# Kernel optimization log

Hardware: AMD Instinct MI355X
Metric: run time of the kernel (lower is better)

## Reference

```python
import jax, jax.numpy as jnp
import numpy as np

B, S, D, H = 2, 2048, 2048, 16
HD = D // H
RESIDUAL_SCALE = 1.0
EPS = 1e-6


def setup_inputs() -> dict:
    key = jax.random.key(0)
    ks = jax.random.split(key, 6)
    x = jax.random.normal(ks[0], (B, S, D), jnp.float32)
    # rotary tables: emb = cat(freqs, freqs), shape [S, HD]
    inv_freq = 1.0 / (10000.0 ** (jnp.arange(0, HD, 2, dtype=jnp.float32) / HD))
    t = jnp.arange(S, dtype=jnp.float32)
    freqs = jnp.einsum('s,f->sf', t, inv_freq)
    emb = jnp.concatenate([freqs, freqs], axis=-1)
    cos, sin = jnp.cos(emb), jnp.sin(emb)
    sc = 0.02
    w_qkv = jax.random.normal(ks[1], (3 * D, D), jnp.float32) * sc
    w_out = jax.random.normal(ks[2], (D, D), jnp.float32) * sc
    w_fc1 = jax.random.normal(ks[3], (4 * D, D), jnp.float32) * sc
    w_fc2 = jax.random.normal(ks[4], (D, 4 * D), jnp.float32) * sc
    g1 = jnp.ones((D,), jnp.float32)
    g2 = jnp.ones((D,), jnp.float32)
    return {'x': x, 'cos': cos, 'sin': sin, 'g1': g1, 'g2': g2,
            'w_qkv': w_qkv, 'w_out': w_out, 'w_fc1': w_fc1, 'w_fc2': w_fc2}


def _rmsnorm(x, g):
    xf = x.astype(jnp.float32)
    norm = jnp.sqrt(jnp.mean(xf * xf, axis=-1, keepdims=True) + EPS)
    return g * (xf / norm)


def _rotate_half(x):
    x1, x2 = jnp.split(x, 2, axis=-1)
    return jnp.concatenate([-x2, x1], axis=-1)


def _rope(t, cos, sin):
    # t: [B, S, H, HD]; cos/sin: [S, HD]
    c = cos[None, :, None, :]
    s = sin[None, :, None, :]
    return t * c + _rotate_half(t) * s


def reference(x, cos, sin, g1, g2, w_qkv, w_out, w_fc1, w_fc2):
    b, s, d = x.shape
    x_skip = x
    h = _rmsnorm(x, g1)
    qkv = (h @ w_qkv.T).reshape(b, s, 3, H, HD)
    q = _rope(qkv[:, :, 0], cos, sin)
    k = _rope(qkv[:, :, 1], cos, sin)
    v = qkv[:, :, 2]  # rotary is identity on v
    scale = 1.0 / jnp.sqrt(jnp.asarray(HD, dtype=q.dtype))
    scores = jnp.einsum('bqhd,bkhd->bhqk', q, k) * scale
    causal = jnp.triu(jnp.ones((s, s), dtype=bool), k=1)
    scores = jnp.where(causal[None, None], -jnp.inf, scores)
    attn = jax.nn.softmax(scores, axis=-1)
    o = jnp.einsum('bhqk,bkhd->bqhd', attn, v).reshape(b, s, d)
    x = x_skip + RESIDUAL_SCALE * (o @ w_out.T)
    x_skip = x
    h = _rmsnorm(x, g2)
    h = jax.nn.gelu(h @ w_fc1.T, approximate=True) @ w_fc2.T
    return x_skip + RESIDUAL_SCALE * h
```

## Files before the change

kernel.cpp:

```cpp
#include <hip/hip_runtime.h>
#include <stdint.h>

typedef unsigned short u16;
typedef u16 u16x4 __attribute__((ext_vector_type(4)));
typedef u16 u16x8 __attribute__((ext_vector_type(8)));
typedef __bf16 bf16x8 __attribute__((ext_vector_type(8)));
typedef float f32x4 __attribute__((ext_vector_type(4)));
typedef float f32x16 __attribute__((ext_vector_type(16)));

#define MFMA16 __builtin_amdgcn_mfma_f32_16x16x32_bf16
#define MFMA32 __builtin_amdgcn_mfma_f32_32x32x16_bf16

static __device__ __forceinline__ float b2f(u16 u) {
    union { unsigned int i; float f; } v; v.i = ((unsigned int)u) << 16; return v.f;
}
static __device__ __forceinline__ u16 f2b(float f) {
    union { float f; unsigned int i; } v; v.f = f;
    unsigned int r = (v.i + 0x7fffu + ((v.i >> 16) & 1u)) >> 16;
    return (u16)r;
}
static __device__ __forceinline__ unsigned pk2(float lo, float hi) {
    union { __bf16 b[2]; unsigned u; } t;
    t.b[0] = (__bf16)lo; t.b[1] = (__bf16)hi; return t.u;
}
static __device__ __forceinline__ void gload_lds16(const void* g, void* l) {
    __builtin_amdgcn_global_load_lds((__attribute__((address_space(1))) void*)g,
                                     (__attribute__((address_space(3))) void*)l,
                                     16, 0, 0);
}

__global__ __launch_bounds__(256) void cvt_k(const float* __restrict__ in,
                                             u16* __restrict__ out, long n) {
    long i = ((long)blockIdx.x * 256 + threadIdx.x) * 4;
    if (i >= n) return;
    float4 v = *(const float4*)(in + i);
    u16x4 o; o[0] = f2b(v.x); o[1] = f2b(v.y); o[2] = f2b(v.z); o[3] = f2b(v.w);
    *(u16x4*)(out + i) = o;
}

__global__ __launch_bounds__(256) void addred_k(float* __restrict__ xout,
                                                const float* __restrict__ p0,
                                                const float* __restrict__ p1) {
    long i = ((long)blockIdx.x * 256 + threadIdx.x) * 4;
    float4 a = *(const float4*)(xout + i);
    float4 b = *(const float4*)(p0 + i);
    float4 c = *(const float4*)(p1 + i);
    a.x += b.x + c.x; a.y += b.y + c.y; a.z += b.z + c.z; a.w += b.w + c.w;
    *(float4*)(xout + i) = a;
}

__global__ __launch_bounds__(256) void rmsnorm_k(const float* __restrict__ x,
                                                 const float* __restrict__ g,
                                                 u16* __restrict__ out) {
    const long row = blockIdx.x;
    const int tid = threadIdx.x;
    const float* xr = x + row * 2048;
    float4 a = *(const float4*)(xr + tid * 4);
    float4 b = *(const float4*)(xr + 1024 + tid * 4);
    float ss = a.x*a.x + a.y*a.y + a.z*a.z + a.w*a.w
             + b.x*b.x + b.y*b.y + b.z*b.z + b.w*b.w;
    #pragma unroll
    for (int d = 1; d < 64; d <<= 1) ss += __shfl_xor(ss, d);
    __shared__ float red[4];
    if ((tid & 63) == 0) red[tid >> 6] = ss;
    __syncthreads();
    float tot = red[0] + red[1] + red[2] + red[3];
    float rinv = rsqrtf(tot * (1.0f / 2048.0f) + 1e-6f);
    float4 g0 = *(const float4*)(g + tid * 4);
    float4 g1 = *(const float4*)(g + 1024 + tid * 4);
    u16x4 o0, o1;
    o0[0] = f2b(a.x * g0.x * rinv); o0[1] = f2b(a.y * g0.y * rinv);
    o0[2] = f2b(a.z * g0.z * rinv); o0[3] = f2b(a.w * g0.w * rinv);
    o1[0] = f2b(b.x * g1.x * rinv); o1[1] = f2b(b.y * g1.y * rinv);
    o1[2] = f2b(b.z * g1.z * rinv); o1[3] = f2b(b.w * g1.w * rinv);
    *(u16x4*)(out + row * 2048 + tid * 4) = o0;
    *(u16x4*)(out + row * 2048 + 1024 + tid * 4) = o1;
}

__global__ __launch_bounds__(256) void rope_k(u16* __restrict__ qkv,
                                              const float* __restrict__ cosb,
                                              const float* __restrict__ sinb) {
    long idx = (long)blockIdx.x * 256 + threadIdx.x;
    int d = (int)(idx & 15) * 4;
    int h = (int)((idx >> 4) & 15);
    int which = (int)((idx >> 8) & 1);
    long row = idx >> 9;
    int s = (int)(row & 2047);
    u16* base = qkv + row * 6144 + which * 2048 + h * 128;
    u16x4 ua = *(u16x4*)(base + d);
    u16x4 ub = *(u16x4*)(base + d + 64);
    float4 c4 = *(const float4*)(cosb + (long)s * 128 + d);
    float4 s4 = *(const float4*)(sinb + (long)s * 128 + d);
    float cc[4] = {c4.x, c4.y, c4.z, c4.w};
    float sn[4] = {s4.x, s4.y, s4.z, s4.w};
    float scale = (which == 0) ? 0.08838834764831845f : 1.0f;
    u16x4 oa, ob;
    #pragma unroll
    for (int j = 0; j < 4; ++j) {
        float a = b2f(ua[j]), b = b2f(ub[j]);
        oa[j] = f2b((a * cc[j] - b * sn[j]) * scale);
        ob[j] = f2b((b * cc[j] + a * sn[j]) * scale);
    }
    *(u16x4*)(base + d) = oa;
    *(u16x4*)(base + d + 64) = ob;
}

__global__ __launch_bounds__(256) void vtrans_k(const u16* __restrict__ qkv,
                                                u16* __restrict__ vt) {
    __shared__ u16 t[128 * 65];
    const int bh = blockIdx.y, b = bh >> 4, h = bh & 15;
    const int s0 = blockIdx.x * 64;
    const int tid = threadIdx.x;
    #pragma unroll
    for (int it = 0; it < 4; ++it) {
        int flat = it * 256 + tid;
        int sl = flat >> 4, slot = flat & 15;
        u16x8 v = *(const u16x8*)(qkv + (long)(b * 2048 + s0 + sl) * 6144 + 4096 +
                                  h * 128 + slot * 8);
        #pragma unroll
        for (int j = 0; j < 8; ++j) t[(slot * 8 + j) * 65 + sl] = v[j];
    }
    __syncthreads();
    #pragma unroll
    for (int it = 0; it < 4; ++it) {
        int flat = it * 256 + tid;
        int d = flat >> 3, sg = flat & 7;
        u16x8 v;
        #pragma unroll
        for (int j = 0; j < 8; ++j) v[j] = t[d * 65 + sg * 8 + j];
        *(u16x8*)(vt + ((long)bh * 128 + d) * 2048 + s0 + sg * 8) = v;
    }
}

template <int EPI>
__global__ __launch_bounds__(256) void gemm_bt(const u16* __restrict__ A,
                                               const u16* __restrict__ W,
                                               int M, int N, int K,
                                               u16* outb, float* outf,
                                               const float* res) {
    __shared__ u16 As[128 * 32];
    __shared__ u16 Bs[128 * 32];
    const int tid = threadIdx.x;
    const int wave = tid >> 6, lane = tid & 63;
    const int wr = wave >> 1, wc = wave & 1;
    const int bm = blockIdx.y, bn = blockIdx.x;
    const int l4 = lane >> 2;
    const int c8 = (lane & 3) * 8;
    const long arow0 = (long)bm * 128;
    const long brow0 = (long)bn * 128;

    f32x4 acc[4][4];
    #pragma unroll
    for (int m = 0; m < 4; ++m)
        #pragma unroll
        for (int n = 0; n < 4; ++n) acc[m][n] = (f32x4){0.f, 0.f, 0.f, 0.f};

    const int nk = K >> 5;
    for (int kt = 0; kt < nk; ++kt) {
        __syncthreads();
        #pragma unroll
        for (int p = 0; p < 2; ++p) {
            int row = p * 64 + wave * 16 + l4;
            const u16* ga = A + (arow0 + row) * (long)K + kt * 32 + c8;
            gload_lds16(ga, (char*)As + p * 4096 + wave * 1024);
            const u16* gb = W + (brow0 + row) * (long)K + kt * 32 + c8;
            gload_lds16(gb, (char*)Bs + p * 4096 + wave * 1024);
        }
        __syncthreads();
        bf16x8 af[4], bfr[4];
        #pragma unroll
        for (int m = 0; m < 4; ++m)
            af[m] = *(const bf16x8*)((const char*)As +
                     (wr * 64 + m * 16 + (lane & 15)) * 64 + (lane >> 4) * 16);
        #pragma unroll
        for (int n = 0; n < 4; ++n)
            bfr[n] = *(const bf16x8*)((const char*)Bs +
                     (wc * 64 + n * 16 + (lane & 15)) * 64 + (lane >> 4) * 16);
        #pragma unroll
        for (int m = 0; m < 4; ++m)
            #pragma unroll
            for (int n = 0; n < 4; ++n)
                acc[m][n] = MFMA16(af[m], bfr[n], acc[m][n], 0, 0, 0);
    }

    const int rb = bm * 128 + wr * 64 + ((lane >> 4) << 2);
    const int cb = bn * 128 + wc * 64 + (lane & 15);
    #pragma unroll
    for (int m = 0; m < 4; ++m) {
        #pragma unroll
        for (int r = 0; r < 4; ++r) {
            long row = rb + m * 16 + r;
            #pragma unroll
            for (int n = 0; n < 4; ++n) {
                long col = cb + n * 16;
                float v = acc[m][n][r];
                if (EPI == 1) {
                    outf[row * N + col] = res[row * N + col] + v;
                } else if (EPI == 2) {
                    float u = 0.7978845608028654f * v * (1.0f + 0.044715f * v * v);
                    float e = __expf(2.0f * u);
                    float t = 1.0f - 2.0f / (e + 1.0f);
                    outb[row * N + col] = f2b(0.5f * v * (1.0f + t));
                } else {
                    outb[row * N + col] = f2b(v);
                }
            }
        }
    }
}

#define DS_A(BUF, SM, KK) (*(const bf16x8*)(ldsb + (BUF)*32768 + \
        ((((SM)*2) + (KK)) << 10) + rin64 + cst2))
#define DS_B(BUF, SN, KK) (*(const bf16x8*)(ldsb + 65536 + (BUF)*32768 + \
        ((((SN)*2) + (KK)) << 10) + rin64 + cst2))
#define STAGE_A(BUF, SK, KT) do { \
    gload_lds16(sA0 + ((long)(KT)*64 + (SK)*32), ldsb + (BUF)*32768 + (w4 + (SK))*1024); \
    gload_lds16(sA1 + ((long)(KT)*64 + (SK)*32), ldsb + (BUF)*32768 + (w4 + 2 + (SK))*1024); \
} while (0)
#define STAGE_B(BUF, SK, KT) do { \
    gload_lds16(sB0 + ((long)(KT)*64 + (SK)*32), ldsb + 65536 + (BUF)*32768 + (w4 + (SK))*1024); \
    gload_lds16(sB1 + ((long)(KT)*64 + (SK)*32), ldsb + 65536 + (BUF)*32768 + (w4 + 2 + (SK))*1024); \
} while (0)
#define PHASE(BUF, MH, KK, RDB, STAGE_STMT, VM) do { \
    bf16x8 af[4]; \
    _Pragma("unroll") \
    for (int m = 0; m < 4; ++m) af[m] = DS_A(BUF, wr8 + (MH)*4 + m, KK); \
    if (RDB) { \
        bfr[0] = DS_B(BUF, wc4 + 0, KK); bfr[1] = DS_B(BUF, wc4 + 1, KK); \
        bfr[2] = DS_B(BUF, wc4 + 2, KK); bfr[3] = DS_B(BUF, wc4 + 3, KK); \
    } \
    STAGE_STMT; \
    if (VM) { asm volatile("s_waitcnt vmcnt(6)" ::: "memory"); } \
    __builtin_amdgcn_sched_barrier(0); \
    __builtin_amdgcn_s_barrier(); \
    __builtin_amdgcn_sched_barrier(0); \
    __builtin_amdgcn_s_setprio(1); \
    _Pragma("unroll") \
    for (int m = 0; m < 4; ++m) \
        _Pragma("unroll") \
        for (int n = 0; n < 4; ++n) \
            acc[(MH)*4 + m][n] = MFMA16(af[m], bfr[n], acc[(MH)*4 + m][n], 0, 0, 0); \
    __builtin_amdgcn_s_setprio(0); \
    __builtin_amdgcn_sched_barrier(0); \
    __builtin_amdgcn_s_barrier(); \
    __builtin_amdgcn_sched_barrier(0); \
} while (0)

template <int EPI>
__global__ __launch_bounds__(512, 2) void gemm256(const u16* __restrict__ A,
                                                  const u16* __restrict__ W,
                                                  int M, int N, int K,
                                                  u16* outb, float* outf,
                                                  const float* res, int ksplit) {
    __shared__ u16 lds_[65536];
    char* ldsb = (char*)lds_;
    const int tid = threadIdx.x;
    const int w = tid >> 6, l = tid & 63;
    const int w4 = w * 4;
    const int wr8 = (w >> 2) * 8;
    const int wc4 = (w & 3) * 4;
    const int rin64 = (l & 15) * 64;
    const int cst2 = ((((l >> 4) * 8) ^ (((l >> 3) & 1) << 4)) << 1);

    const int nbn = N >> 8;
    const int nwg = gridDim.x;
    const int cpx = nwg >> 3;
    const int bid = blockIdx.x;
    int wg = (bid & 7) * cpx + (bid >> 3);
    int kseg = 0;
    int Keff = K;
    if (ksplit == 2) {
        kseg = wg & 1;
        wg >>= 1;
        Keff = K >> 1;
    }
    const int bm = wg / nbn, bn = wg % nbn;
    const u16* Ab = A + (long)kseg * Keff;
    const u16* Wb = W + (long)kseg * Keff;

    const int r4 = l >> 2;
    const int clog = ((l & 3) * 8) ^ (((r4 >> 3) & 1) << 4);
    const u16* sA0 = Ab + ((long)bm * 256 + (w * 2 + 0) * 16 + r4) * K + clog;
    const u16* sA1 = Ab + ((long)bm * 256 + (w * 2 + 1) * 16 + r4) * K + clog;
    const u16* sB0 = Wb + ((long)bn * 256 + (w * 2 + 0) * 16 + r4) * K + clog;
    const u16* sB1 = Wb + ((long)bn * 256 + (w * 2 + 1) * 16 + r4) * K + clog;

    f32x4 acc[8][4];
    #pragma unroll
    for (int m = 0; m < 8; ++m)
        #pragma unroll
        for (int n = 0; n < 4; ++n) acc[m][n] = (f32x4){0.f, 0.f, 0.f, 0.f};
    bf16x8 bfr[4];

    const int nkt = Keff >> 6;
    const int niter = nkt >> 1;

    STAGE_B(0, 0, 0); STAGE_A(0, 0, 0); STAGE_B(0, 1, 0); STAGE_A(0, 1, 0);
    STAGE_B(1, 0, 1); STAGE_A(1, 0, 1); STAGE_B(1, 1, 1);
    asm volatile("s_waitcnt vmcnt(6)" ::: "memory");
    __builtin_amdgcn_sched_barrier(0);
    __builtin_amdgcn_s_barrier();
    __builtin_amdgcn_sched_barrier(0);

    for (int it = 0; it < niter; ++it) {
        const int t = it * 2;
        const int t1 = t + 1;
        const int t2 = (t + 2 < nkt) ? t + 2 : nkt - 1;
        const int t3 = (t + 3 < nkt) ? t + 3 : nkt - 1;
        PHASE(0, 0, 0, 1, STAGE_A(1, 1, t1), 0);
        PHASE(0, 1, 0, 0, STAGE_B(0, 0, t2), 0);
        PHASE(0, 0, 1, 1, STAGE_A(0, 0, t2), 0);
        PHASE(0, 1, 1, 0, STAGE_B(0, 1, t2), 1);
        PHASE(1, 0, 0, 1, STAGE_A(0, 1, t2), 0);
        PHASE(1, 1, 0, 0, STAGE_B(1, 0, t3), 0);
        PHASE(1, 0, 1, 1, STAGE_A(1, 0, t3), 0);
        PHASE(1, 1, 1, 0, STAGE_B(1, 1, t3), 1);
    }
    asm volatile("s_waitcnt vmcnt(0)" ::: "memory");

    const int rb = bm * 256 + (wr8 >> 3) * 128 + ((l >> 4) << 2);
    const int cb = bn * 256 + (w & 3) * 64 + (l & 15);
    float* pf = (EPI == 3) ? (outf + (long)kseg * M * N) : outf;
    #pragma unroll
    for (int m = 0; m < 8; ++m) {
        #pragma unroll
        for (int r = 0; r < 4; ++r) {
            long row = rb + m * 16 + r;
            #pragma unroll
            for (int n = 0; n < 4; ++n) {
                long col = cb + n * 16;
                float v = acc[m][n][r];
                if (EPI == 1) {
                    pf[row * N + col] = res[row * N + col] + v;
                } else if (EPI == 2) {
                    float u = 0.7978845608028654f * v * (1.0f + 0.044715f * v * v);
                    float e = __expf(2.0f * u);
                    float tgl = 1.0f - 2.0f / (e + 1.0f);
                    outb[row * N + col] = f2b(0.5f * v * (1.0f + tgl));
                } else if (EPI == 3) {
                    pf[row * N + col] = v;
                } else {
                    outb[row * N + col] = f2b(v);
                }
            }
        }
    }
}

struct AttnState {
    f32x16 acc[4];
    float m_i, l_i;
};

template <bool DIAG>
static __device__ __forceinline__ void attn_tile(
    int kv0, int qg, int wave, int l31, int hi,
    const u16* __restrict__ Ks, const u16* __restrict__ Vt,
    const bf16x8 (&qf)[8], AttnState& st)
{
    const bool do_g1 = !(DIAG && wave == 0);
    f32x16 sacc0, sacc1;
    #pragma unroll
    for (int r = 0; r < 16; ++r) { sacc0[r] = 0.f; sacc1[r] = 0.f; }

    #pragma unroll
    for (int dsl = 0; dsl < 8; ++dsl) {
        int slot = dsl * 2 + hi;
        int kv = l31;
        int sw = (slot & 8) | ((slot & 7) ^ (kv & 7));
        bf16x8 kf = *(const bf16x8*)(Ks + kv * 128 + sw * 8);
        sacc0 = MFMA32(kf, qf[dsl], sacc0, 0, 0, 0);
    }
    if (do_g1) {
        #pragma unroll
        for (int dsl = 0; dsl < 8; ++dsl) {
            int slot = dsl * 2 + hi;
            int kv = 32 + l31;
            int sw = (slot & 8) | ((slot & 7) ^ (kv & 7));
            bf16x8 kf = *(const bf16x8*)(Ks + kv * 128 + sw * 8);
            sacc1 = MFMA32(kf, qf[dsl], sacc1, 0, 0, 0);
        }
    }

    float sv[2][16];
    #pragma unroll
    for (int r = 0; r < 16; ++r) {
        sv[0][r] = sacc0[r];
        sv[1][r] = do_g1 ? sacc1[r] : -INFINITY;
    }
    if (DIAG) {
        #pragma unroll
        for (int g = 0; g < 2; ++g)
            #pragma unroll
            for (int r = 0; r < 16; ++r) {
                int kvg = kv0 + g * 32 + ((r & 3) + 8 * (r >> 2) + 4 * hi);
                if (kvg > qg) sv[g][r] = -INFINITY;
            }
    }

    float mx = sv[0][0];
    #pragma unroll
    for (int r = 1; r < 16; ++r) mx = fmaxf(mx, sv[0][r]);
    #pragma unroll
    for (int r = 0; r < 16; ++r) mx = fmaxf(mx, sv[1][r]);
    mx = fmaxf(mx, __shfl_xor(mx, 32));

    bool defer = __all(mx <= st.m_i + 8.0f);
    if (!defer) {
        float mnew = fmaxf(st.m_i, mx);
        float f = __expf(st.m_i - mnew);
        st.l_i *= f;
        #pragma unroll
        for (int dblk = 0; dblk < 4; ++dblk)
            #pragma unroll
            for (int r = 0; r < 16; ++r) st.acc[dblk][r] *= f;
        st.m_i = mnew;
    }

    float ssum = 0.f;
    #pragma unroll
    for (int g = 0; g < 2; ++g)
        #pragma unroll
        for (int r = 0; r < 16; ++r) {
            float e = __expf(sv[g][r] - st.m_i);
            sv[g][r] = e;
            ssum += e;
        }
    ssum += __shfl_xor(ssum, 32);
    st.l_i += ssum;

    unsigned w[2][4][2];
    #pragma unroll
    for (int g = 0; g < 2; ++g)
        #pragma unroll
        for (int q4 = 0; q4 < 4; ++q4) {
            w[g][q4][0] = pk2(sv[g][4 * q4 + 0], sv[g][4 * q4 + 1]);
            w[g][q4][1] = pk2(sv[g][4 * q4 + 2], sv[g][4 * q4 + 3]);
        }
    bf16x8 pfrag[4];
    #pragma unroll
    for (int ks = 0; ks < 4; ++ks) {
        int g = ks >> 1, h2 = ks & 1;
        unsigned o0 = hi ? w[g][2 * h2 + 1][0] : w[g][2 * h2][0];
        unsigned o1 = hi ? w[g][2 * h2 + 1][1] : w[g][2 * h2][1];
        unsigned t0 = hi ? w[g][2 * h2][0] : w[g][2 * h2 + 1][0];
        unsigned t1 = hi ? w[g][2 * h2][1] : w[g][2 * h2 + 1][1];
        unsigned s0v = __shfl_xor(t0, 32);
        unsigned s1v = __shfl_xor(t1, 32);
        union { unsigned u[4]; bf16x8 v; } cv;
        cv.u[0] = hi ? s0v : o0;
        cv.u[1] = hi ? s1v : o1;
        cv.u[2] = hi ? o0 : s0v;
        cv.u[3] = hi ? o1 : s1v;
        pfrag[ks] = cv.v;
    }

    #pragma unroll
    for (int dblk = 0; dblk < 4; ++dblk) {
        int d = dblk * 32 + l31;
        #pragma unroll
        for (int ks = 0; ks < 4; ++ks) {
            if (ks >= 2 && !do_g1) continue;
            int slot = ks * 2 + hi;
            bf16x8 vf = *(const bf16x8*)(Vt + d * 64 + (slot ^ (d & 7)) * 8);
            st.acc[dblk] = MFMA32(vf, pfrag[ks], st.acc[dblk], 0, 0, 0);
        }
    }
}

__global__ __launch_bounds__(128) void attn2_k(const u16* __restrict__ qkv,
                                               const u16* __restrict__ vt,
                                               u16* __restrict__ out) {
    const int bh = blockIdx.y;
    const int b = bh >> 4, h = bh & 15;
    const int qb = blockIdx.x;
    const int q0 = qb * 64;
    const int tid = threadIdx.x, wave = tid >> 6, lane = tid & 63;
    const int l31 = lane & 31, hi = lane >> 5;
    const int brow = b * 2048;
    __shared__ u16 Ks_lds[64 * 128];
    __shared__ u16 Vt_lds[128 * 64];

    bf16x8 qf[8];
    {
        const u16* qp = qkv + (long)(brow + q0 + wave * 32 + l31) * 6144 +
                        h * 128 + hi * 8;
        #pragma unroll
        for (int dsl = 0; dsl < 8; ++dsl) qf[dsl] = *(const bf16x8*)(qp + dsl * 16);
    }

    AttnState st;
    st.m_i = -INFINITY; st.l_i = 0.f;
    #pragma unroll
    for (int dblk = 0; dblk < 4; ++dblk)
        #pragma unroll
        for (int r = 0; r < 16; ++r) st.acc[dblk][r] = 0.f;

    const int qg = q0 + wave * 32 + l31;

    for (int t = 0; t <= qb; ++t) {
        const int kv0 = t * 64;
        __syncthreads();
        #pragma unroll
        for (int i = 0; i < 8; ++i) {
            int kv = wave * 32 + i * 4 + (lane >> 4);
            int slot = lane & 15;
            int sw = (slot & 8) | ((slot & 7) ^ (kv & 7));
            const u16* src = qkv + (long)(brow + kv0 + kv) * 6144 + 2048 +
                             h * 128 + sw * 8;
            gload_lds16(src, (char*)Ks_lds + (wave * 32 + i * 4) * 256);
        }
        #pragma unroll
        for (int i = 0; i < 8; ++i) {
            int d = wave * 64 + i * 8 + (lane >> 3);
            int slot = lane & 7;
            int sw = slot ^ (d & 7);
            const u16* src = vt + ((long)bh * 128 + d) * 2048 + kv0 + sw * 8;
            gload_lds16(src, (char*)Vt_lds + (wave * 64 + i * 8) * 128);
        }
        __syncthreads();
        if (t < qb)
            attn_tile<false>(kv0, qg, wave, l31, hi, Ks_lds, Vt_lds, qf, st);
        else
            attn_tile<true>(kv0, qg, wave, l31, hi, Ks_lds, Vt_lds, qf, st);
    }

    float inv = 1.0f / st.l_i;
    long orow = (long)(brow + q0 + wave * 32 + l31);
    #pragma unroll
    for (int dblk = 0; dblk < 4; ++dblk)
        #pragma unroll
        for (int rq = 0; rq < 4; ++rq) {
            u16x4 o4;
            #pragma unroll
            for (int m = 0; m < 4; ++m) o4[m] = f2b(st.acc[dblk][rq * 4 + m] * inv);
            int d = dblk * 32 + 8 * rq + 4 * hi;
            *(u16x4*)(out + orow * 2048 + h * 128 + d) = o4;
        }
}

extern "C" void kernel_launch(void* const* d_in, const int* in_sizes, int n_in,
                              void* d_out, int out_size, void* d_ws, size_t ws_size,
                              hipStream_t stream) {
    const float* x     = (const float*)d_in[0];
    const float* cosb  = (const float*)d_in[1];
    const float* sinb  = (const float*)d_in[2];
    const float* g1    = (const float*)d_in[3];
    const float* g2    = (const float*)d_in[4];
    const float* w_qkv = (const float*)d_in[5];
    const float* w_out = (const float*)d_in[6];
    const float* w_fc1 = (const float*)d_in[7];
    const float* w_fc2 = (const float*)d_in[8];

    char* ws = (char*)d_ws;
    u16* wqkv_b = (u16*)(ws);
    u16* wout_b = (u16*)(ws + 25165824);
    u16* wfc1_b = (u16*)(ws + 33554432);
    u16* wfc2_b = (u16*)(ws + 67108864);
    u16* h_b    = (u16*)(ws + 100663296);
    u16* qkv_b  = (u16*)(ws + 117440512);
    u16* attn_b = (u16*)(ws + 167772160);
    u16* vt_b   = h_b;
    u16* hg_b   = qkv_b;
    float* part = (float*)ws;
    float* xout = (float*)d_out;

    cvt_k<<<12288, 256, 0, stream>>>(w_qkv, wqkv_b, 12582912L);
    cvt_k<<<4096, 256, 0, stream>>>(w_out, wout_b, 4194304L);
    cvt_k<<<16384, 256, 0, stream>>>(w_fc1, wfc1_b, 16777216L);
    cvt_k<<<16384, 256, 0, stream>>>(w_fc2, wfc2_b, 16777216L);

    rmsnorm_k<<<4096, 256, 0, stream>>>(x, g1, h_b);
    gemm256<0><<<384, 512, 0, stream>>>(h_b, wqkv_b, 4096, 6144, 2048,
                                        qkv_b, nullptr, nullptr, 1);
    rope_k<<<8192, 256, 0, stream>>>(qkv_b, cosb, sinb);
    vtrans_k<<<dim3(32, 32), 256, 0, stream>>>(qkv_b, vt_b);
    attn2_k<<<dim3(32, 32), 128, 0, stream>>>(qkv_b, vt_b, attn_b);
    gemm_bt<1><<<dim3(16, 32), 256, 0, stream>>>(attn_b, wout_b, 4096, 2048, 2048,
                                                 nullptr, xout, x);
    rmsnorm_k<<<4096, 256, 0, stream>>>(xout, g2, h_b);
    gemm256<2><<<512, 512, 0, stream>>>(h_b, wfc1_b, 4096, 8192, 2048,
                                        hg_b, nullptr, nullptr, 1);
    gemm256<3><<<256, 512, 0, stream>>>(hg_b, wfc2_b, 4096, 2048, 8192,
                                        nullptr, part, nullptr, 2);
    addred_k<<<8192, 256, 0, stream>>>(xout, part, part + 8388608);
}
```

Before: 686.7 us.

## Route out-projection through split-K gemm256 and group tiles for L2 reuse

Replaces the simple 128x128 gemm_bt for the attention output projection with the pipelined 256x256 gemm256 kernel using a two-way K split. The partial results go to scratch and a new reduction kernel adds them to the residual. It also changes the workgroup-to-tile mapping in gemm256 to group eight row tiles together, aiming for better L2 reuse of weight tiles. This costs an extra reduction pass and extra fp32 partial traffic.

```diff
diff --git a/kernel.cpp b/kernel.cpp
--- a/kernel.cpp
+++ b/kernel.cpp
@@ -47,6 +47,18 @@
     float4 c = *(const float4*)(p1 + i);
     a.x += b.x + c.x; a.y += b.y + c.y; a.z += b.z + c.z; a.w += b.w + c.w;
     *(float4*)(xout + i) = a;
+}
+
+__global__ __launch_bounds__(256) void addred2_k(float* __restrict__ xout,
+                                                 const float* __restrict__ x,
+                                                 const float* __restrict__ p0,
+                                                 const float* __restrict__ p1) {
+    long i = ((long)blockIdx.x * 256 + threadIdx.x) * 4;
+    float4 r = *(const float4*)(x + i);
+    float4 b = *(const float4*)(p0 + i);
+    float4 c = *(const float4*)(p1 + i);
+    r.x += b.x + c.x; r.y += b.y + c.y; r.z += b.z + c.z; r.w += b.w + c.w;
+    *(float4*)(xout + i) = r;
 }
 
 __global__ __launch_bounds__(256) void rmsnorm_k(const float* __restrict__ x,
@@ -129,83 +141,6 @@
         #pragma unroll
         for (int j = 0; j < 8; ++j) v[j] = t[d * 65 + sg * 8 + j];
         *(u16x8*)(vt + ((long)bh * 128 + d) * 2048 + s0 + sg * 8) = v;
-    }
-}
-
-template <int EPI>
-__global__ __launch_bounds__(256) void gemm_bt(const u16* __restrict__ A,
-                                               const u16* __restrict__ W,
-                                               int M, int N, int K,
-                                               u16* outb, float* outf,
-                                               const float* res) {
-    __shared__ u16 As[128 * 32];
-    __shared__ u16 Bs[128 * 32];
-    const int tid = threadIdx.x;
-    const int wave = tid >> 6, lane = tid & 63;
-    const int wr = wave >> 1, wc = wave & 1;
-    const int bm = blockIdx.y, bn = blockIdx.x;
-    const int l4 = lane >> 2;
-    const int c8 = (lane & 3) * 8;
-    const long arow0 = (long)bm * 128;
-    const long brow0 = (long)bn * 128;
-
-    f32x4 acc[4][4];
-    #pragma unroll
-    for (int m = 0; m < 4; ++m)
-        #pragma unroll
-        for (int n = 0; n < 4; ++n) acc[m][n] = (f32x4){0.f, 0.f, 0.f, 0.f};
-
-    const int nk = K >> 5;
-    for (int kt = 0; kt < nk; ++kt) {
-        __syncthreads();
-        #pragma unroll
-        for (int p = 0; p < 2; ++p) {
-            int row = p * 64 + wave * 16 + l4;
-            const u16* ga = A + (arow0 + row) * (long)K + kt * 32 + c8;
-            gload_lds16(ga, (char*)As + p * 4096 + wave * 1024);
-            const u16* gb = W + (brow0 + row) * (long)K + kt * 32 + c8;
-            gload_lds16(gb, (char*)Bs + p * 4096 + wave * 1024);
-        }
-        __syncthreads();
-        bf16x8 af[4], bfr[4];
-        #pragma unroll
-        for (int m = 0; m < 4; ++m)
-            af[m] = *(const bf16x8*)((const char*)As +
-                     (wr * 64 + m * 16 + (lane & 15)) * 64 + (lane >> 4) * 16);
-        #pragma unroll
-        for (int n = 0; n < 4; ++n)
-            bfr[n] = *(const bf16x8*)((const char*)Bs +
-                     (wc * 64 + n * 16 + (lane & 15)) * 64 + (lane >> 4) * 16);
-        #pragma unroll
-        for (int m = 0; m < 4; ++m)
-            #pragma unroll
-            for (int n = 0; n < 4; ++n)
-                acc[m][n] = MFMA16(af[m], bfr[n], acc[m][n], 0, 0, 0);
-    }
-
-    const int rb = bm * 128 + wr * 64 + ((lane >> 4) << 2);
-    const int cb = bn * 128 + wc * 64 + (lane & 15);
-    #pragma unroll
-    for (int m = 0; m < 4; ++m) {
-        #pragma unroll
-        for (int r = 0; r < 4; ++r) {
-            long row = rb + m * 16 + r;
-            #pragma unroll
-            for (int n = 0; n < 4; ++n) {
-                long col = cb + n * 16;
-                float v = acc[m][n][r];
-                if (EPI == 1) {
-                    outf[row * N + col] = res[row * N + col] + v;
-                } else if (EPI == 2) {
-                    float u = 0.7978845608028654f * v * (1.0f + 0.044715f * v * v);
-                    float e = __expf(2.0f * u);
-                    float t = 1.0f - 2.0f / (e + 1.0f);
-                    outb[row * N + col] = f2b(0.5f * v * (1.0f + t));
-                } else {
-                    outb[row * N + col] = f2b(v);
-                }
-            }
-        }
     }
 }
 
@@ -263,6 +198,7 @@
     const int cst2 = ((((l >> 4) * 8) ^ (((l >> 3) & 1) << 4)) << 1);
 
     const int nbn = N >> 8;
+    const int nbm = M >> 8;
     const int nwg = gridDim.x;
     const int cpx = nwg >> 3;
     const int bid = blockIdx.x;
@@ -274,7 +210,13 @@
         wg >>= 1;
         Keff = K >> 1;
     }
-    const int bm = wg / nbn, bn = wg % nbn;
+    const int grp = 8 * nbn;
+    const int g8 = wg / grp;
+    const int rem = wg - g8 * grp;
+    const int bm0 = g8 * 8;
+    const int gmh = (nbm - bm0 < 8) ? (nbm - bm0) : 8;
+    const int bn = rem / gmh;
+    const int bm = bm0 + rem % gmh;
     const u16* Ab = A + (long)kseg * Keff;
     const u16* Wb = W + (long)kseg * Keff;
 
@@ -563,6 +505,7 @@
     u16* vt_b   = h_b;
     u16* hg_b   = qkv_b;
     float* part = (float*)ws;
+    float* pop  = (float*)(ws + 100663296);
     float* xout = (float*)d_out;
 
     cvt_k<<<12288, 256, 0, stream>>>(w_qkv, wqkv_b, 12582912L);
@@ -576,8 +519,9 @@
     rope_k<<<8192, 256, 0, stream>>>(qkv_b, cosb, sinb);
     vtrans_k<<<dim3(32, 32), 256, 0, stream>>>(qkv_b, vt_b);
     attn2_k<<<dim3(32, 32), 128, 0, stream>>>(qkv_b, vt_b, attn_b);
-    gemm_bt<1><<<dim3(16, 32), 256, 0, stream>>>(attn_b, wout_b, 4096, 2048, 2048,
-                                                 nullptr, xout, x);
+    gemm256<3><<<256, 512, 0, stream>>>(attn_b, wout_b, 4096, 2048, 2048,
+                                        nullptr, pop, nullptr, 2);
+    addred2_k<<<8192, 256, 0, stream>>>(xout, x, pop, pop + 8388608);
     rmsnorm_k<<<4096, 256, 0, stream>>>(xout, g2, h_b);
     gemm256<2><<<512, 512, 0, stream>>>(h_b, wfc1_b, 4096, 8192, 2048,
                                         hg_b, nullptr, nullptr, 1);
```

After: 677.0 us. About the same (-1.4%).
